# Kernel optimization log

Hardware: AMD Instinct MI355X
Metric: run time of the kernel (lower is better)

## Reference

```python
import jax, jax.numpy as jnp
import numpy as np
import math

# Model dims (see shape_source)
BATCH, SEQ, HH, WW = 32, 128, 32, 32   # x: (B, seq_len, H, W); L = H*W = 1024
D_MODEL = 1024                          # hidden_dim
N2 = 4                                  # n=8 -> 4 complex S4D modes
L_MAX = 64                              # SSM kernel length (l_max)


def _layernorm(x, gamma, beta, eps=1e-5):
    mu = jnp.mean(x, axis=-1, keepdims=True)
    var = jnp.var(x, axis=-1, keepdims=True)
    return (x - mu) * jax.lax.rsqrt(var + eps) * gamma + beta


def setup_inputs() -> dict:
    key = jax.random.key(0)
    ks = jax.random.split(key, 12)
    d_in = SEQ  # d_input = d_output = seq_len
    inp = {
        "x": jax.random.normal(ks[0], (BATCH, SEQ, HH, WW), dtype=jnp.float32),
        # encoder Linear(d_input -> d_model)
        "W_enc": jax.random.normal(ks[1], (d_in, D_MODEL), dtype=jnp.float32) / math.sqrt(d_in),
        "b_enc": jnp.zeros((D_MODEL,), dtype=jnp.float32),
        # S4D SSM parameters (per d_model channel, N2 complex modes)
        "log_dt": (jax.random.uniform(ks[2], (D_MODEL,), dtype=jnp.float32)
                   * (math.log(0.1) - math.log(0.001)) + math.log(0.001)),
        "A_log_real": jnp.full((D_MODEL, N2), math.log(0.5), dtype=jnp.float32),
        "A_imag": jnp.broadcast_to(math.pi * jnp.arange(N2, dtype=jnp.float32), (D_MODEL, N2)).copy(),
        "C_real": jax.random.normal(ks[3], (D_MODEL, N2), dtype=jnp.float32) * 0.5,
        "C_imag": jax.random.normal(ks[4], (D_MODEL, N2), dtype=jnp.float32) * 0.5,
        "D": jax.random.normal(ks[5], (D_MODEL,), dtype=jnp.float32),
        # position-wise GLU mixing Linear(d_model -> 2*d_model)
        "W_glu": jax.random.normal(ks[6], (D_MODEL, 2 * D_MODEL), dtype=jnp.float32) / math.sqrt(D_MODEL),
        "b_glu": jnp.zeros((2 * D_MODEL,), dtype=jnp.float32),
        "ln_gamma": jnp.ones((D_MODEL,), dtype=jnp.float32),
        "ln_beta": jnp.zeros((D_MODEL,), dtype=jnp.float32),
        # decoder Linear(d_model -> d_output)
        "W_dec": jax.random.normal(ks[7], (D_MODEL, d_in), dtype=jnp.float32) / math.sqrt(D_MODEL),
        "b_dec": jnp.zeros((d_in,), dtype=jnp.float32),
    }
    return inp


def reference(x, W_enc, b_enc, log_dt, A_log_real, A_imag, C_real, C_imag, D,
              W_glu, b_glu, ln_gamma, ln_beta, W_dec, b_dec):
    Bsz, S, Hh, Ww = x.shape
    L = Hh * Ww
    u = x.reshape(Bsz, S, L)                                  # (B, d_input, L)
    # encoder applied per position along L
    h = jnp.einsum('bdl,de->ble', u, W_enc) + b_enc           # (B, L, d_model)

    # ---- S4D kernel (ZOH discretization, B=1, diagonal A) ----
    dt = jnp.exp(log_dt)                                      # (d,)
    A = -jnp.exp(A_log_real) + 1j * A_imag                    # (d, n2) complex
    Cc = C_real + 1j * C_imag
    dtA = A * dt[:, None]                                     # (d, n2)
    Bd = (jnp.exp(dtA) - 1.0) / A                             # ZOH input matrix
    t = jnp.arange(L_MAX)
    vand = jnp.exp(dtA[:, :, None] * t)                       # (d, n2, l_max)
    K = 2.0 * jnp.einsum('dn,dnl->dl', Cc * Bd, vand).real    # (d, l_max)

    # ---- causal FFT convolution along L + skip D*u ----
    z = jnp.swapaxes(h, 1, 2)                                 # (B, d, L)
    n_fft = L + L_MAX
    y = jnp.fft.irfft(jnp.fft.rfft(z, n=n_fft) * jnp.fft.rfft(K, n=n_fft), n=n_fft)[..., :L]
    y = y + D[:, None] * z                                    # (B, d, L)

    # ---- block: GELU -> GLU mixing -> residual -> LayerNorm ----
    y = jax.nn.gelu(jnp.swapaxes(y, 1, 2))                    # (B, L, d)
    g = y @ W_glu + b_glu                                     # (B, L, 2d)
    g = g[..., :D_MODEL] * jax.nn.sigmoid(g[..., D_MODEL:])
    h = _layernorm(h + g, ln_gamma, ln_beta)                  # (B, L, d)

    out = h @ W_dec + b_dec                                   # (B, L, d_output)
    out = jnp.swapaxes(out, 1, 2).reshape(Bsz, S, Hh, Ww)
    return out
```

## Files before the change

### kernel.cpp

```cpp
#include <hip/hip_runtime.h>
#include <hip/hip_bf16.h>
#include <math.h>

#define B_ 32
#define S_ 128
#define L_ 1024
#define D_ 1024

typedef unsigned short u16;
typedef __attribute__((ext_vector_type(8))) __bf16 bf16x8;
typedef __attribute__((ext_vector_type(4))) float f32x4;

__device__ __forceinline__ float bf2f(u16 u) {
    return __uint_as_float(((unsigned)u) << 16);
}
__device__ __forceinline__ u16 f2bf(float f) {
    unsigned u = __float_as_uint(f);
    u += 0x7FFF + ((u >> 16) & 1);
    return (u16)(u >> 16);
}
__device__ __forceinline__ float gelu_tanh(float x) {
    float x3 = x * x * x;
    float t = tanhf(0.7978845608028654f * (x + 0.044715f * x3));
    return 0.5f * x * (1.0f + t);
}
__device__ __forceinline__ float sigmoidf(float x) {
    return 1.0f / (1.0f + expf(-x));
}
__device__ __forceinline__ void gld16(const void* g, void* l) {
    __builtin_amdgcn_global_load_lds((const __attribute__((address_space(1))) void*)g,
                                     (__attribute__((address_space(3))) void*)l, 16, 0, 0);
}

__global__ __launch_bounds__(256) void k_ssmk(
        const float* __restrict__ log_dt, const float* __restrict__ Alr,
        const float* __restrict__ Aim, const float* __restrict__ Cr,
        const float* __restrict__ Ci, float* __restrict__ Kt) {
    int tid = blockIdx.x * 256 + threadIdx.x;
    int d = tid & (D_ - 1);
    int j = tid >> 10;
    float dt = expf(log_dt[d]);
    float acc = 0.f;
    #pragma unroll
    for (int n = 0; n < 4; ++n) {
        float ar = -expf(Alr[d * 4 + n]);
        float ai = Aim[d * 4 + n];
        float wr = ar * dt, wi = ai * dt;
        float ew = expf(wr);
        float sw, cw; sincosf(wi, &sw, &cw);
        float ur = ew * cw - 1.0f, ui = ew * sw;
        float inv = 1.0f / (ar * ar + ai * ai);
        float bdr = (ur * ar + ui * ai) * inv;
        float bdi = (ui * ar - ur * ai) * inv;
        float cr = Cr[d * 4 + n], ci = Ci[d * 4 + n];
        float cbr = cr * bdr - ci * bdi;
        float cbi = cr * bdi + ci * bdr;
        float ej = expf(wr * (float)j);
        float sj, cj; sincosf(wi * (float)j, &sj, &cj);
        acc += 2.0f * ej * (cbr * cj - cbi * sj);
    }
    Kt[j * D_ + d] = acc;
}

__global__ __launch_bounds__(256) void k_tcast(
        const float* __restrict__ src0, u16* __restrict__ dst0, int R, int C) {
    __shared__ float tile[64][65];
    const float* src = src0 + (size_t)blockIdx.z * R * C;
    u16* dst = dst0 + (size_t)blockIdx.z * R * C;
    int c0 = blockIdx.x * 64;
    int r0 = blockIdx.y * 64;
    int t = threadIdx.x;
    #pragma unroll
    for (int p = 0; p < 4; ++p) {
        int fid = p * 256 + t;
        int rr = fid >> 4, cc = (fid & 15) * 4;
        float4 v = *(const float4*)&src[(size_t)(r0 + rr) * C + c0 + cc];
        tile[rr][cc + 0] = v.x; tile[rr][cc + 1] = v.y;
        tile[rr][cc + 2] = v.z; tile[rr][cc + 3] = v.w;
    }
    __syncthreads();
    #pragma unroll
    for (int p = 0; p < 4; ++p) {
        int fid = p * 256 + t;
        int rr = fid >> 4, cc = (fid & 15) * 4;
        ushort4 o;
        o.x = f2bf(tile[cc + 0][rr]);
        o.y = f2bf(tile[cc + 1][rr]);
        o.z = f2bf(tile[cc + 2][rr]);
        o.w = f2bf(tile[cc + 3][rr]);
        *(ushort4*)&dst[(size_t)(c0 + rr) * R + r0 + cc] = o;
    }
}

__global__ __launch_bounds__(256) void k_enc_mfma(
        const u16* __restrict__ xb, const u16* __restrict__ WeT,
        const float* __restrict__ be, u16* __restrict__ hb) {
    __shared__ u16 As[128 * 128];
    __shared__ u16 Bs[128 * 128];
    int t = threadIdx.x;
    int lane = t & 63, wid = t >> 6;
    int wr = wid & 1, wc = wid >> 1;
    int orig = blockIdx.x;
    int wgid = (orig & 7) * 256 + (orig >> 3);
    int m0 = (wgid >> 3) * 128;
    int e0 = (wgid & 7) * 128;

    #pragma unroll
    for (int c = 0; c < 8; ++c) {
        int ch = wid * 8 + c;
        int r = ch * 4 + (lane >> 4);
        int g = (lane & 15) ^ (r & 15);
        gld16(&xb[(size_t)(m0 + r) * 128 + g * 8], &As[ch * 512]);
        gld16(&WeT[(size_t)(e0 + r) * 128 + g * 8], &Bs[ch * 512]);
    }
    int co4[4];
    #pragma unroll
    for (int kh = 0; kh < 4; ++kh)
        co4[kh] = ((((lane >> 4) + kh * 4) ^ (lane & 15)) * 8);
    int arow[4], brow[4];
    #pragma unroll
    for (int i = 0; i < 4; ++i) arow[i] = (wr * 64 + i * 16 + (lane & 15)) * 128;
    #pragma unroll
    for (int q = 0; q < 4; ++q) brow[q] = (wc * 64 + q * 16 + (lane & 15)) * 128;

    __syncthreads();
    f32x4 acc[4][4] = {};
    #pragma unroll
    for (int kh = 0; kh < 4; ++kh) {
        bf16x8 af[4], bfr[4];
        #pragma unroll
        for (int i = 0; i < 4; ++i) af[i] = *(const bf16x8*)&As[arow[i] + co4[kh]];
        #pragma unroll
        for (int q = 0; q < 4; ++q) bfr[q] = *(const bf16x8*)&Bs[brow[q] + co4[kh]];
        __builtin_amdgcn_s_setprio(1);
        #pragma unroll
        for (int i = 0; i < 4; ++i)
            #pragma unroll
            for (int q = 0; q < 4; ++q)
                acc[i][q] = __builtin_amdgcn_mfma_f32_16x16x32_bf16(af[i], bfr[q], acc[i][q], 0, 0, 0);
        __builtin_amdgcn_s_setprio(0);
    }
    #pragma unroll
    for (int q = 0; q < 4; ++q) {
        int e = e0 + wc * 64 + q * 16 + (lane & 15);
        float bias = be[e];
        #pragma unroll
        for (int i = 0; i < 4; ++i) {
            #pragma unroll
            for (int r = 0; r < 4; ++r) {
                int m = m0 + wr * 64 + i * 16 + (lane >> 4) * 4 + r;
                hb[(size_t)m * 1024 + e] = f2bf(acc[i][q][r] + bias);
            }
        }
    }
}

__global__ __launch_bounds__(256) void k_conv(
        const u16* __restrict__ hb, const float* __restrict__ Kt,
        const float* __restrict__ Dv, u16* __restrict__ yg) {
    __shared__ float hs[128][64];
    int b = blockIdx.z;
    int l0 = blockIdx.y * 64;
    int d0 = blockIdx.x * 64;
    int t = threadIdx.x;
    int dl = t & 63, lg = t >> 6;
    #pragma unroll
    for (int p = 0; p < 8; ++p) {
        int fid = p * 256 + t;
        int r = fid >> 4, c4 = fid & 15;
        int l = l0 - 64 + r;
        float4 v = make_float4(0.f, 0.f, 0.f, 0.f);
        if (l >= 0) {
            ushort4 u = *(const ushort4*)&hb[((size_t)b * 1024 + l) * 1024 + d0 + c4 * 4];
            v = make_float4(bf2f(u.x), bf2f(u.y), bf2f(u.z), bf2f(u.w));
        }
        *(float4*)&hs[r][c4 * 4] = v;
    }
    float kr[64];
    #pragma unroll
    for (int j = 0; j < 64; ++j) kr[j] = Kt[j * 1024 + d0 + dl];
    float Dd = Dv[d0 + dl];
    __syncthreads();
    float acc[16] = {};
    int rbase = lg * 16 + 1;
    #pragma unroll
    for (int s = 0; s < 15; ++s) {
        float hv = hs[rbase + s][dl];
        #pragma unroll
        for (int i = 0; i <= 14; ++i)
            if (i <= s) acc[i] = fmaf(kr[i + 63 - s], hv, acc[i]);
    }
    #pragma unroll
    for (int s = 15; s < 64; ++s) {
        float hv = hs[rbase + s][dl];
        #pragma unroll
        for (int i = 0; i < 16; ++i)
            acc[i] = fmaf(kr[i + 63 - s], hv, acc[i]);
    }
    #pragma unroll
    for (int s = 64; s < 79; ++s) {
        float hv = hs[rbase + s][dl];
        #pragma unroll
        for (int i = 1; i < 16; ++i)
            if (i >= s - 63) acc[i] = fmaf(kr[i + 63 - s], hv, acc[i]);
    }
    #pragma unroll
    for (int i = 0; i < 16; ++i) {
        int l = l0 + lg * 16 + i;
        float z = hs[64 + lg * 16 + i][dl];
        float y = acc[i] + Dd * z;
        yg[((size_t)b * 1024 + l) * 1024 + d0 + dl] = f2bf(gelu_tanh(y));
    }
}

__global__ __launch_bounds__(256) void k_glu_mfma(
        const u16* __restrict__ yg, const u16* __restrict__ WgT,
        const float* __restrict__ bg, u16* __restrict__ hb) {
    __shared__ u16 As[2][8192];
    __shared__ u16 Bs[2][8192];
    int t = threadIdx.x;
    int lane = t & 63, wid = t >> 6;
    int wr = wid & 1, wc = wid >> 1;

    int orig = blockIdx.x;
    int wgid = (orig & 7) * 512 + (orig >> 3);
    int m0 = (wgid >> 4) * 128;
    int p0 = (wgid & 15) * 64;

    int gsrc = (((lane & 7) ^ (lane >> 3)) * 8);
    int rA[4], nB[4];
    #pragma unroll
    for (int c = 0; c < 4; ++c) {
        int r = (wid * 4 + c) * 8 + (lane >> 3);
        rA[c] = m0 + r;
        int pairIdx = ((r >> 5) << 4) | (r & 15);
        int half = (r >> 4) & 1;
        nB[c] = half * 1024 + p0 + pairIdx;
    }
    int co[2];
    co[0] = (((lane >> 4) + 0) ^ (lane & 7)) * 8;
    co[1] = (((lane >> 4) + 4) ^ (lane & 7)) * 8;
    int arow[4], brow[4];
    #pragma unroll
    for (int i = 0; i < 4; ++i) arow[i] = (wr * 64 + i * 16 + (lane & 15)) * 64;
    #pragma unroll
    for (int q = 0; q < 4; ++q) brow[q] = (wc * 64 + q * 16 + (lane & 15)) * 64;

    f32x4 acc[4][4] = {};
    #pragma unroll
    for (int c = 0; c < 4; ++c) {
        int ch = wid * 4 + c;
        gld16(&yg[(size_t)rA[c] * 1024 + gsrc], &As[0][ch * 512]);
        gld16(&WgT[(size_t)nB[c] * 1024 + gsrc], &Bs[0][ch * 512]);
    }
    __syncthreads();
    int cur = 0;
    for (int kt = 0; kt < 16; ++kt) {
        if (kt < 15) {
            int k0 = (kt + 1) * 64;
            #pragma unroll
            for (int c = 0; c < 4; ++c) {
                int ch = wid * 4 + c;
                gld16(&yg[(size_t)rA[c] * 1024 + k0 + gsrc], &As[cur ^ 1][ch * 512]);
                gld16(&WgT[(size_t)nB[c] * 1024 + k0 + gsrc], &Bs[cur ^ 1][ch * 512]);
            }
        }
        #pragma unroll
        for (int kh = 0; kh < 2; ++kh) {
            bf16x8 af[4], bfr[4];
            #pragma unroll
            for (int i = 0; i < 4; ++i) af[i] = *(const bf16x8*)&As[cur][arow[i] + co[kh]];
            #pragma unroll
            for (int q = 0; q < 4; ++q) bfr[q] = *(const bf16x8*)&Bs[cur][brow[q] + co[kh]];
            __builtin_amdgcn_s_setprio(1);
            #pragma unroll
            for (int i = 0; i < 4; ++i)
                #pragma unroll
                for (int q = 0; q < 4; ++q)
                    acc[i][q] = __builtin_amdgcn_mfma_f32_16x16x32_bf16(af[i], bfr[q], acc[i][q], 0, 0, 0);
            __builtin_amdgcn_s_setprio(0);
        }
        __syncthreads();
        cur ^= 1;
    }
    #pragma unroll
    for (int i = 0; i < 4; ++i) {
        #pragma unroll
        for (int qq = 0; qq < 2; ++qq) {
            int pair = (wc * 2 + qq) * 16 + (lane & 15);
            int col = p0 + pair;
            float b1v = bg[col];
            float b2v = bg[1024 + col];
            #pragma unroll
            for (int r = 0; r < 4; ++r) {
                int m = m0 + wr * 64 + i * 16 + (lane >> 4) * 4 + r;
                float g1 = acc[i][qq * 2][r] + b1v;
                float g2 = acc[i][qq * 2 + 1][r] + b2v;
                size_t idx = (size_t)m * 1024 + col;
                float hf = bf2f(hb[idx]);
                hb[idx] = f2bf(hf + g1 * sigmoidf(g2));
            }
        }
    }
}

__global__ __launch_bounds__(256) void k_ln(
        u16* __restrict__ hb, const float* __restrict__ gamma,
        const float* __restrict__ beta) {
    int row = blockIdx.x;
    int t = threadIdx.x;
    size_t base = (size_t)row * 1024;
    ushort4 u = *(const ushort4*)&hb[base + t * 4];
    float v0 = bf2f(u.x), v1 = bf2f(u.y), v2 = bf2f(u.z), v3 = bf2f(u.w);
    float s = v0 + v1 + v2 + v3;
    float s2 = v0 * v0 + v1 * v1 + v2 * v2 + v3 * v3;
    #pragma unroll
    for (int off = 32; off > 0; off >>= 1) {
        s += __shfl_down(s, off);
        s2 += __shfl_down(s2, off);
    }
    __shared__ float rs[4], rs2[4];
    int wid = t >> 6, lane = t & 63;
    if (lane == 0) { rs[wid] = s; rs2[wid] = s2; }
    __syncthreads();
    float ts = rs[0] + rs[1] + rs[2] + rs[3];
    float ts2 = rs2[0] + rs2[1] + rs2[2] + rs2[3];
    float mean = ts * (1.0f / 1024.0f);
    float var = ts2 * (1.0f / 1024.0f) - mean * mean;
    float rstd = rsqrtf(var + 1e-5f);
    float4 gm = *(const float4*)&gamma[t * 4];
    float4 bt = *(const float4*)&beta[t * 4];
    ushort4 o;
    o.x = f2bf((v0 - mean) * rstd * gm.x + bt.x);
    o.y = f2bf((v1 - mean) * rstd * gm.y + bt.y);
    o.z = f2bf((v2 - mean) * rstd * gm.z + bt.z);
    o.w = f2bf((v3 - mean) * rstd * gm.w + bt.w);
    *(ushort4*)&hb[base + t * 4] = o;
}

__global__ __launch_bounds__(256) void k_dec_mfma(
        const u16* __restrict__ hb, const u16* __restrict__ WdT,
        const float* __restrict__ bd, float* __restrict__ out) {
    __shared__ __align__(16) char smem[65536];
    u16* As = (u16*)smem;
    u16* Bs = (u16*)(smem + 32768);
    float* Ts = (float*)smem;
    int t = threadIdx.x;
    int lane = t & 63, wid = t >> 6;
    int wr = wid & 1, wc = wid >> 1;
    int m0 = blockIdx.x * 128;
    int bb = m0 >> 10, l0 = m0 & 1023;

    int gsrc = (((lane & 7) ^ (lane >> 3)) * 8);
    int rr4[4];
    #pragma unroll
    for (int c = 0; c < 4; ++c) rr4[c] = (wid * 4 + c) * 8 + (lane >> 3);
    int co[2];
    co[0] = (((lane >> 4) + 0) ^ (lane & 7)) * 8;
    co[1] = (((lane >> 4) + 4) ^ (lane & 7)) * 8;
    int arow[4], brow[4];
    #pragma unroll
    for (int i = 0; i < 4; ++i) arow[i] = (wr * 64 + i * 16 + (lane & 15)) * 64;
    #pragma unroll
    for (int q = 0; q < 4; ++q) brow[q] = (wc * 64 + q * 16 + (lane & 15)) * 64;

    f32x4 acc[4][4] = {};
    #pragma unroll
    for (int c = 0; c < 4; ++c) {
        int ch = wid * 4 + c;
        gld16(&hb[(size_t)(m0 + rr4[c]) * 1024 + gsrc], &As[0 * 8192 + ch * 512]);
        gld16(&WdT[(size_t)rr4[c] * 1024 + gsrc], &Bs[0 * 8192 + ch * 512]);
    }
    __syncthreads();
    int cur = 0;
    for (int kt = 0; kt < 16; ++kt) {
        if (kt < 15) {
            int k0 = (kt + 1) * 64;
            #pragma unroll
            for (int c = 0; c < 4; ++c) {
                int ch = wid * 4 + c;
                gld16(&hb[(size_t)(m0 + rr4[c]) * 1024 + k0 + gsrc], &As[(cur ^ 1) * 8192 + ch * 512]);
                gld16(&WdT[(size_t)rr4[c] * 1024 + k0 + gsrc], &Bs[(cur ^ 1) * 8192 + ch * 512]);
            }
        }
        #pragma unroll
        for (int kh = 0; kh < 2; ++kh) {
            bf16x8 af[4], bfr[4];
            #pragma unroll
            for (int i = 0; i < 4; ++i) af[i] = *(const bf16x8*)&As[cur * 8192 + arow[i] + co[kh]];
            #pragma unroll
            for (int q = 0; q < 4; ++q) bfr[q] = *(const bf16x8*)&Bs[cur * 8192 + brow[q] + co[kh]];
            __builtin_amdgcn_s_setprio(1);
            #pragma unroll
            for (int i = 0; i < 4; ++i)
                #pragma unroll
                for (int q = 0; q < 4; ++q)
                    acc[i][q] = __builtin_amdgcn_mfma_f32_16x16x32_bf16(af[i], bfr[q], acc[i][q], 0, 0, 0);
            __builtin_amdgcn_s_setprio(0);
        }
        __syncthreads();
        cur ^= 1;
    }
    __syncthreads();
    #pragma unroll
    for (int ro = 0; ro < 2; ++ro) {
        if (wc == ro) {
            #pragma unroll
            for (int i = 0; i < 4; ++i)
                #pragma unroll
                for (int q = 0; q < 4; ++q) {
                    int sl = q * 16 + (lane & 15);
                    float bias = bd[ro * 64 + sl];
                    #pragma unroll
                    for (int r = 0; r < 4; ++r) {
                        int ml = wr * 64 + i * 16 + (lane >> 4) * 4 + r;
                        Ts[sl * 132 + ml] = acc[i][q][r] + bias;
                    }
                }
        }
        __syncthreads();
        #pragma unroll
        for (int p = 0; p < 8; ++p) {
            int fid = p * 256 + t;
            int sl = fid >> 5, c = (fid & 31) * 4;
            float4 v = *(const float4*)&Ts[sl * 132 + c];
            *(float4*)&out[(size_t)bb * 131072 + (size_t)(ro * 64 + sl) * 1024 + l0 + c] = v;
        }
        __syncthreads();
    }
}

extern "C" void kernel_launch(void* const* d_in, const int* in_sizes, int n_in,
                              void* d_out, int out_size, void* d_ws, size_t ws_size,
                              hipStream_t stream) {
    (void)in_sizes; (void)n_in; (void)out_size; (void)ws_size;
    const float* x   = (const float*)d_in[0];
    const float* We  = (const float*)d_in[1];
    const float* be  = (const float*)d_in[2];
    const float* ldt = (const float*)d_in[3];
    const float* Alr = (const float*)d_in[4];
    const float* Aim = (const float*)d_in[5];
    const float* Cr  = (const float*)d_in[6];
    const float* Ci  = (const float*)d_in[7];
    const float* Dv  = (const float*)d_in[8];
    const float* Wg  = (const float*)d_in[9];
    const float* bg  = (const float*)d_in[10];
    const float* gam = (const float*)d_in[11];
    const float* bet = (const float*)d_in[12];
    const float* Wd  = (const float*)d_in[13];
    const float* bd  = (const float*)d_in[14];
    float* out = (float*)d_out;

    u16* hb = (u16*)d_ws;
    u16* yg = hb + 33554432ull;
    float* Kt = (float*)(yg + 33554432ull);
    u16* WgT = (u16*)(Kt + 65536);
    u16* WdT = WgT + 2097152ull;
    u16* WeT = WdT + 131072ull;
    u16* xb  = yg;

    k_tcast<<<dim3(32, 16, 1), 256, 0, stream>>>(Wg, WgT, 1024, 2048);
    k_tcast<<<dim3(2, 16, 1), 256, 0, stream>>>(Wd, WdT, 1024, 128);
    k_tcast<<<dim3(16, 2, 1), 256, 0, stream>>>(We, WeT, 128, 1024);
    k_tcast<<<dim3(16, 2, 32), 256, 0, stream>>>(x, xb, 128, 1024);
    k_ssmk<<<256, 256, 0, stream>>>(ldt, Alr, Aim, Cr, Ci, Kt);
    k_enc_mfma<<<2048, 256, 0, stream>>>(xb, WeT, be, hb);
    k_conv<<<dim3(16, 16, 32), 256, 0, stream>>>(hb, Kt, Dv, yg);
    k_glu_mfma<<<4096, 256, 0, stream>>>(yg, WgT, bg, hb);
    k_ln<<<32768, 256, 0, stream>>>(hb, gam, bet);
    k_dec_mfma<<<256, 256, 0, stream>>>(hb, WdT, bd, out);
}
```

Before: 365.4 us.

## Enlarge GLU GEMM tile to 256x256 with 8 waves and interleaved staging

Replaces the 128x128 (64 output pair) GLU GEMM block with a 512-thread block covering 256 rows by 256 weight columns. Each wave computes a 128x64 sub-tile, which doubles per-block operand reuse and cuts global and L2 traffic per FLOP. Global-to-LDS prefetch of the next K tile is split into four chunks interleaved with MFMA clusters, coordinated by explicit vmcnt waits and barriers. It costs more registers (64 accumulators per lane) and 128KB of LDS per block, and the extra barriers may limit overlap.

After: 343.8 us. -5.9%, faster.

```diff
diff --git a/kernel.cpp b/kernel.cpp
--- a/kernel.cpp
+++ b/kernel.cpp
@@ -213,95 +213,130 @@
     }
 }
 
-__global__ __launch_bounds__(256) void k_glu_mfma(
+__global__ __launch_bounds__(512, 2) void k_glu256(
         const u16* __restrict__ yg, const u16* __restrict__ WgT,
         const float* __restrict__ bg, u16* __restrict__ hb) {
-    __shared__ u16 As[2][8192];
-    __shared__ u16 Bs[2][8192];
+    __shared__ u16 Asm[2][16384];
+    __shared__ u16 Bsm[2][16384];
     int t = threadIdx.x;
     int lane = t & 63, wid = t >> 6;
-    int wr = wid & 1, wc = wid >> 1;
+    int wr = wid >> 2, wc = wid & 3;
 
     int orig = blockIdx.x;
-    int wgid = (orig & 7) * 512 + (orig >> 3);
-    int m0 = (wgid >> 4) * 128;
-    int p0 = (wgid & 15) * 64;
-
-    int gsrc = (((lane & 7) ^ (lane >> 3)) * 8);
-    int rA[4], nB[4];
-    #pragma unroll
-    for (int c = 0; c < 4; ++c) {
-        int r = (wid * 4 + c) * 8 + (lane >> 3);
-        rA[c] = m0 + r;
-        int pairIdx = ((r >> 5) << 4) | (r & 15);
-        int half = (r >> 4) & 1;
-        nB[c] = half * 1024 + p0 + pairIdx;
-    }
-    int co[2];
-    co[0] = (((lane >> 4) + 0) ^ (lane & 7)) * 8;
-    co[1] = (((lane >> 4) + 4) ^ (lane & 7)) * 8;
-    int arow[4], brow[4];
-    #pragma unroll
-    for (int i = 0; i < 4; ++i) arow[i] = (wr * 64 + i * 16 + (lane & 15)) * 64;
-    #pragma unroll
-    for (int q = 0; q < 4; ++q) brow[q] = (wc * 64 + q * 16 + (lane & 15)) * 64;
-
-    f32x4 acc[4][4] = {};
-    #pragma unroll
-    for (int c = 0; c < 4; ++c) {
-        int ch = wid * 4 + c;
-        gld16(&yg[(size_t)rA[c] * 1024 + gsrc], &As[0][ch * 512]);
-        gld16(&WgT[(size_t)nB[c] * 1024 + gsrc], &Bs[0][ch * 512]);
-    }
-    __syncthreads();
+    int wgid = (orig & 7) * 128 + (orig >> 3);
+    int m0 = (wgid >> 3) * 256;
+    int p0g = (wgid & 7) * 128;
+
+    int rl = lane >> 3;
+    int gsw = ((lane & 7) ^ rl) * 8;
+    int ch0 = wid * 2, ch1 = wid * 2 + 1;
+    int rA0 = (ch0 >> 3) * 128 + (ch0 & 7) * 8 + rl;
+    int rA1 = (ch1 >> 3) * 128 + (ch1 & 7) * 8 + rl;
+    int dA0 = ((ch0 >> 3) * 128 + (ch0 & 7) * 8) * 64;
+    int dA1 = ((ch1 >> 3) * 128 + (ch1 & 7) * 8) * 64;
+    int rB0 = (ch0 >> 2) * 64 + (ch0 & 3) * 8 + rl;
+    int rB1 = (ch1 >> 2) * 64 + (ch1 & 3) * 8 + rl;
+    int dB0 = ((ch0 >> 2) * 64 + (ch0 & 3) * 8) * 64;
+    int dB1 = ((ch1 >> 2) * 64 + (ch1 & 3) * 8) * 64;
+    int gB0 = ((rB0 >> 4) & 1) * 1024 + p0g + (((rB0 >> 5) << 4) | (rB0 & 15));
+    int gB1 = ((rB1 >> 4) & 1) * 1024 + p0g + (((rB1 >> 5) << 4) | (rB1 & 15));
+
+    int co0 = (((lane >> 4) + 0) ^ (lane & 7)) * 8;
+    int co1 = (((lane >> 4) + 4) ^ (lane & 7)) * 8;
+    int abase = (wr * 128 + (lane & 15)) * 64;
+    int bbase = (wc * 64 + (lane & 15)) * 64;
+
+#define STG_A0(BUF, K0) { gld16(&yg[(size_t)(m0 + rA0) * 1024 + (K0) + gsw], &Asm[BUF][dA0]); \
+                          gld16(&yg[(size_t)(m0 + rA1) * 1024 + (K0) + gsw], &Asm[BUF][dA1]); }
+#define STG_A1(BUF, K0) { gld16(&yg[(size_t)(m0 + rA0 + 64) * 1024 + (K0) + gsw], &Asm[BUF][dA0 + 4096]); \
+                          gld16(&yg[(size_t)(m0 + rA1 + 64) * 1024 + (K0) + gsw], &Asm[BUF][dA1 + 4096]); }
+#define STG_B0(BUF, K0) { gld16(&WgT[(size_t)gB0 * 1024 + (K0) + gsw], &Bsm[BUF][dB0]); \
+                          gld16(&WgT[(size_t)gB1 * 1024 + (K0) + gsw], &Bsm[BUF][dB1]); }
+#define STG_B1(BUF, K0) { gld16(&WgT[(size_t)(gB0 + 16) * 1024 + (K0) + gsw], &Bsm[BUF][dB0 + 2048]); \
+                          gld16(&WgT[(size_t)(gB1 + 16) * 1024 + (K0) + gsw], &Bsm[BUF][dB1 + 2048]); }
+#define RD_A(MH) { _Pragma("unroll") for (int i = 0; i < 4; ++i) { \
+        a0[i][0] = *(const bf16x8*)&Ac[abase + (MH) * 4096 + i * 1024 + co0]; \
+        a0[i][1] = *(const bf16x8*)&Ac[abase + (MH) * 4096 + i * 1024 + co1]; } }
+#define RD_B(BB, OFS) { _Pragma("unroll") for (int q = 0; q < 2; ++q) { \
+        BB[q][0] = *(const bf16x8*)&Bc[bbase + (OFS) + q * 1024 + co0]; \
+        BB[q][1] = *(const bf16x8*)&Bc[bbase + (OFS) + q * 1024 + co1]; } }
+#define MFMA_CL(MI, BB, NQ) { __builtin_amdgcn_s_setprio(1); \
+    _Pragma("unroll") for (int i = 0; i < 4; ++i) \
+        _Pragma("unroll") for (int q = 0; q < 2; ++q) { \
+            acc[(MI) * 4 + i][(NQ) + q] = __builtin_amdgcn_mfma_f32_16x16x32_bf16(a0[i][0], BB[q][0], acc[(MI) * 4 + i][(NQ) + q], 0, 0, 0); \
+            acc[(MI) * 4 + i][(NQ) + q] = __builtin_amdgcn_mfma_f32_16x16x32_bf16(a0[i][1], BB[q][1], acc[(MI) * 4 + i][(NQ) + q], 0, 0, 0); } \
+    __builtin_amdgcn_s_setprio(0); }
+
+    f32x4 acc[8][4] = {};
+    bf16x8 a0[4][2], b0[2][2], b1[2][2];
+
+    STG_A0(0, 0); STG_B0(0, 0); STG_B1(0, 0); STG_A1(0, 0);
+
     int cur = 0;
-    for (int kt = 0; kt < 16; ++kt) {
-        if (kt < 15) {
-            int k0 = (kt + 1) * 64;
-            #pragma unroll
-            for (int c = 0; c < 4; ++c) {
-                int ch = wid * 4 + c;
-                gld16(&yg[(size_t)rA[c] * 1024 + k0 + gsrc], &As[cur ^ 1][ch * 512]);
-                gld16(&WgT[(size_t)nB[c] * 1024 + k0 + gsrc], &Bs[cur ^ 1][ch * 512]);
-            }
-        }
-        #pragma unroll
-        for (int kh = 0; kh < 2; ++kh) {
-            bf16x8 af[4], bfr[4];
-            #pragma unroll
-            for (int i = 0; i < 4; ++i) af[i] = *(const bf16x8*)&As[cur][arow[i] + co[kh]];
-            #pragma unroll
-            for (int q = 0; q < 4; ++q) bfr[q] = *(const bf16x8*)&Bs[cur][brow[q] + co[kh]];
-            __builtin_amdgcn_s_setprio(1);
-            #pragma unroll
-            for (int i = 0; i < 4; ++i)
-                #pragma unroll
-                for (int q = 0; q < 4; ++q)
-                    acc[i][q] = __builtin_amdgcn_mfma_f32_16x16x32_bf16(af[i], bfr[q], acc[i][q], 0, 0, 0);
-            __builtin_amdgcn_s_setprio(0);
-        }
-        __syncthreads();
-        cur ^= 1;
-    }
-    #pragma unroll
-    for (int i = 0; i < 4; ++i) {
-        #pragma unroll
-        for (int qq = 0; qq < 2; ++qq) {
-            int pair = (wc * 2 + qq) * 16 + (lane & 15);
-            int col = p0 + pair;
+    for (int kt = 0; kt < 15; ++kt) {
+        const u16* Ac = &Asm[cur][0];
+        const u16* Bc = &Bsm[cur][0];
+        int nxt = cur ^ 1, k1 = (kt + 1) * 64;
+        asm volatile("s_waitcnt vmcnt(2)" ::: "memory");
+        __builtin_amdgcn_s_barrier();
+        RD_A(0); RD_B(b0, 0);
+        STG_A0(nxt, k1);
+        __builtin_amdgcn_s_barrier();
+        MFMA_CL(0, b0, 0);
+        RD_B(b1, 2048);
+        STG_B0(nxt, k1);
+        __builtin_amdgcn_s_barrier();
+        MFMA_CL(0, b1, 2);
+        asm volatile("s_waitcnt vmcnt(4)" ::: "memory");
+        __builtin_amdgcn_s_barrier();
+        RD_A(1);
+        STG_B1(nxt, k1);
+        __builtin_amdgcn_s_barrier();
+        MFMA_CL(1, b0, 0);
+        STG_A1(nxt, k1);
+        __builtin_amdgcn_s_barrier();
+        MFMA_CL(1, b1, 2);
+        cur = nxt;
+    }
+    {
+        const u16* Ac = &Asm[cur][0];
+        const u16* Bc = &Bsm[cur][0];
+        asm volatile("s_waitcnt vmcnt(2)" ::: "memory");
+        __builtin_amdgcn_s_barrier();
+        RD_A(0); RD_B(b0, 0);
+        MFMA_CL(0, b0, 0);
+        RD_B(b1, 2048);
+        MFMA_CL(0, b1, 2);
+        asm volatile("s_waitcnt vmcnt(0)" ::: "memory");
+        __builtin_amdgcn_s_barrier();
+        RD_A(1);
+        MFMA_CL(1, b0, 0);
+        MFMA_CL(1, b1, 2);
+    }
+    #pragma unroll
+    for (int i = 0; i < 8; ++i) {
+        #pragma unroll
+        for (int tt = 0; tt < 2; ++tt) {
+            int col = p0g + (wc * 2 + tt) * 16 + (lane & 15);
             float b1v = bg[col];
             float b2v = bg[1024 + col];
             #pragma unroll
             for (int r = 0; r < 4; ++r) {
-                int m = m0 + wr * 64 + i * 16 + (lane >> 4) * 4 + r;
-                float g1 = acc[i][qq * 2][r] + b1v;
-                float g2 = acc[i][qq * 2 + 1][r] + b2v;
+                int m = m0 + wr * 128 + i * 16 + (lane >> 4) * 4 + r;
                 size_t idx = (size_t)m * 1024 + col;
-                float hf = bf2f(hb[idx]);
-                hb[idx] = f2bf(hf + g1 * sigmoidf(g2));
+                float g1 = acc[i][tt * 2][r] + b1v;
+                float g2 = acc[i][tt * 2 + 1][r] + b2v;
+                hb[idx] = f2bf(bf2f(hb[idx]) + g1 * sigmoidf(g2));
             }
         }
     }
+#undef STG_A0
+#undef STG_A1
+#undef STG_B0
+#undef STG_B1
+#undef RD_A
+#undef RD_B
+#undef MFMA_CL
 }
 
 __global__ __launch_bounds__(256) void k_ln(
@@ -466,7 +501,7 @@
     k_ssmk<<<256, 256, 0, stream>>>(ldt, Alr, Aim, Cr, Ci, Kt);
     k_enc_mfma<<<2048, 256, 0, stream>>>(xb, WeT, be, hb);
     k_conv<<<dim3(16, 16, 32), 256, 0, stream>>>(hb, Kt, Dv, yg);
-    k_glu_mfma<<<4096, 256, 0, stream>>>(yg, WgT, bg, hb);
+    k_glu256<<<1024, 512, 0, stream>>>(yg, WgT, bg, hb);
     k_ln<<<32768, 256, 0, stream>>>(hb, gam, bet);
     k_dec_mfma<<<256, 256, 0, stream>>>(hb, WdT, bd, out);
 }
```
